# Performance work log

Measured on AMD Instinct MI355X. Metric: run time of the kernel, lower is better.

Reference implementation:

```python
import jax, jax.numpy as jnp
import numpy as np

D = 128          # data_dim
H = 512          # hidden_dim
K = 10           # num_bins
BATCH = 32768
BOUND = 5.0
MINW = 1e-3
MINH = 1e-3
MIND = 1e-3
MASK = np.array([1.0] * (D // 2) + [0.0] * (D // 2), dtype=np.float32)
TIDX = np.where(MASK == 0)[0]  # transformed dims (static)


def _rqs_forward(x, uw, uh, ud):
    # x: [B, T]; uw/uh: [B, T, K]; ud: [B, T, K-1]
    w = jax.nn.softmax(uw, axis=-1)
    w = MINW + (1.0 - MINW * K) * w
    cw = jnp.pad(jnp.cumsum(w, axis=-1), ((0, 0), (0, 0), (1, 0)))
    cw = 2.0 * BOUND * cw - BOUND
    cw = cw.at[..., 0].set(-BOUND).at[..., -1].set(BOUND)
    w = cw[..., 1:] - cw[..., :-1]

    h = jax.nn.softmax(uh, axis=-1)
    h = MINH + (1.0 - MINH * K) * h
    ch = jnp.pad(jnp.cumsum(h, axis=-1), ((0, 0), (0, 0), (1, 0)))
    ch = 2.0 * BOUND * ch - BOUND
    ch = ch.at[..., 0].set(-BOUND).at[..., -1].set(BOUND)
    h = ch[..., 1:] - ch[..., :-1]

    d = MIND + jax.nn.softplus(ud)
    d = jnp.pad(d, ((0, 0), (0, 0), (1, 1)), constant_values=1.0)  # [B,T,K+1]

    inside = (x >= -BOUND) & (x <= BOUND)
    xc = jnp.clip(x, -BOUND, BOUND)  # avoid NaN for outside values

    # searchsorted(cw, x, right=True) - 1, clamped to [0, K-1]
    bin_idx = jnp.clip(jnp.sum(cw <= xc[..., None], axis=-1) - 1, 0, K - 1)

    def gat(a, idx):
        return jnp.take_along_axis(a, idx[..., None], axis=-1)[..., 0]

    wk = gat(w, bin_idx)
    cwk = gat(cw, bin_idx)
    hk = gat(h, bin_idx)
    chk = gat(ch, bin_idx)
    dk = gat(d, bin_idx)
    dk1 = gat(d, bin_idx + 1)

    theta = (xc - cwk) / wk
    s = hk / wk
    tm = theta * (1.0 - theta)
    den = s + (dk + dk1 - 2.0 * s) * tm
    num = hk * (s * theta * theta + dk * tm)
    y = chk + num / den
    ld = jnp.log(s * s * (dk1 * theta * theta + 2.0 * s * tm + dk * (1.0 - theta) ** 2)) - 2.0 * jnp.log(den)

    y = jnp.where(inside, y, x)
    ld = jnp.where(inside, ld, 0.0)
    return y, ld


def setup_inputs() -> dict:
    key = jax.random.key(0)
    ks = jax.random.split(key, 7)
    out_dim = D * (3 * K - 1)
    return {
        "z": jax.random.normal(ks[0], (BATCH, D), dtype=jnp.float32) * 2.0,
        "W1": jax.random.normal(ks[1], (H, D), dtype=jnp.float32) * 0.05,
        "b1": jnp.zeros((H,), dtype=jnp.float32),
        "W2": jax.random.normal(ks[2], (H, H), dtype=jnp.float32) * 0.05,
        "b2": jnp.zeros((H,), dtype=jnp.float32),
        "W3": jax.random.normal(ks[3], (out_dim, H), dtype=jnp.float32) * 0.05,
        "b3": jnp.zeros((out_dim,), dtype=jnp.float32),
    }


def reference(z, W1, b1, W2, b2, W3, b3):
    mask = jnp.asarray(MASK)
    z_a = z * mask
    hdn = jax.nn.relu(z_a @ W1.T + b1)
    hdn = jax.nn.relu(hdn @ W2.T + b2)
    p = (hdn @ W3.T + b3).reshape(-1, D, 3 * K - 1)
    uw, uh, ud = jnp.split(p, [K, 2 * K], axis=-1)

    zb = z[:, TIDX]
    xb, ld = _rqs_forward(zb, uw[:, TIDX], uh[:, TIDX], ud[:, TIDX])

    x = z.at[:, TIDX].set(xb)
    logdet = jnp.sum(ld, axis=1)
    x = jnp.where(jnp.isnan(x) | jnp.isinf(x), 0.0, x)
    logdet = jnp.where(jnp.isnan(logdet) | jnp.isinf(logdet), 0.0, logdet)
    return x, logdet
```

## Files before the change

kernel.cpp:

```cpp
#include <hip/hip_runtime.h>
#include <cmath>

#define BATCH 32768
#define DIM   128
#define HID   512
#define NPAD  2048

typedef __attribute__((ext_vector_type(8))) _Float16 half8;
typedef __attribute__((ext_vector_type(8))) short   short8v;
typedef __attribute__((ext_vector_type(4))) float   f32x4;
typedef unsigned short u16;


__device__ __forceinline__ u16 f2h(float f) {
  _Float16 h = (_Float16)f;
  union { _Float16 h; u16 u; } v; v.h = h; return v.u;
}

__device__ __forceinline__ void async16(const void* g, void* l) {
  __builtin_amdgcn_global_load_lds(
      (const __attribute__((address_space(1))) void*)g,
      (__attribute__((address_space(3))) void*)l, 16, 0, 0);
}

__device__ __forceinline__ int xcd_swz(int bid, int nwg) {
  int cpx = nwg >> 3;
  return (bid & 7) * cpx + (bid >> 3);
}


__global__ __launch_bounds__(256) void prep_all_v8(
    const float* __restrict__ z, const float* __restrict__ W1, const float* __restrict__ W2,
    const float* __restrict__ W3, const float* __restrict__ b3,
    u16* __restrict__ zh, u16* __restrict__ W1h, u16* __restrict__ W2h,
    u16* __restrict__ W3h, float* __restrict__ b3p) {
  const int bid = blockIdx.x;
  if (bid < 1024) {
    int id = bid * 256 + threadIdx.x;
    int l = id & 63, mb = (id >> 6) & 2047, kt = id >> 17;
    int r = mb * 16 + (l & 15);
    int k0 = kt * 32 + ((l >> 4) << 3);
    const float* src = z + (size_t)r * DIM + k0;
    short8v H;
#pragma unroll
    for (int j = 0; j < 8; ++j) H[j] = (short)f2h(src[j]);
    *(short8v*)(zh + (size_t)id * 8) = H;
  } else if (bid < 1168) {
    int id = (bid - 1024) * 256 + threadIdx.x;
    if (id < 4096) {
      int l = id & 63, mb = (id >> 6) & 31, kt = id >> 11;
      int r = mb * 16 + (l & 15);
      int k0 = kt * 32 + ((l >> 4) << 3);
      const float* src = W1 + (size_t)r * DIM + k0;
      short8v H;
#pragma unroll
      for (int j = 0; j < 8; ++j) H[j] = (short)f2h(src[j]);
      *(short8v*)(W1h + (size_t)id * 8) = H;
    } else {
      int id2 = id - 4096;
      int l = id2 & 63, mb = (id2 >> 6) & 31, kt = id2 >> 11;
      int r = mb * 16 + (l & 15);
      int k0 = kt * 32 + ((l >> 4) << 3);
      const float* src = W2 + (size_t)r * HID + k0;
      short8v H;
#pragma unroll
      for (int j = 0; j < 8; ++j) H[j] = (short)f2h(src[j]);
      *(short8v*)(W2h + (size_t)id2 * 8) = H;
    }
  } else if (bid < 1680) {
    int id = (bid - 1168) * 256 + threadIdx.x;
    int l = id & 63, mb = (id >> 6) & 127, kt = id >> 13;
    int n = mb * 16 + (l & 15);
    int k0 = kt * 32 + ((l >> 4) << 3);
    int g = n >> 5, kk = n & 31;
    short8v H;
    if (kk < 29) {
      const float* src = W3 + ((size_t)((g + 64) * 29 + kk)) * HID + k0;
#pragma unroll
      for (int j = 0; j < 8; ++j) H[j] = (short)f2h(src[j]);
    } else {
#pragma unroll
      for (int j = 0; j < 8; ++j) H[j] = 0;
    }
    *(short8v*)(W3h + (size_t)id * 8) = H;
  } else {
    int n = (bid - 1680) * 256 + threadIdx.x;
    int g = n >> 5, kk = n & 31;
    b3p[n] = (kk < 29) ? b3[(g + 64) * 29 + kk] : 0.f;
  }
}


__device__ __forceinline__ void stageA_v8(const u16* __restrict__ A, size_t ab, u16* Lb, int t) {
  async16(A + ab + t * 8,         Lb + t * 8);
  async16(A + ab + (t + 256) * 8, Lb + (t + 256) * 8);
}

template<int NKT>
__device__ __forceinline__ void gemm_mainloop_v8(
    const u16* __restrict__ A, const u16* __restrict__ B,
    int a_rb0, int a_rs16, int b_rb0, int b_rs16,
    u16* LDS, f32x4 acc[4][4]) {
  const int t = threadIdx.x;
  const int lane = t & 63;
  const int wv = t >> 6;
  const int wr = wv >> 1, wc = wv & 1;
  const size_t aStep = (size_t)a_rs16 * 512;
  const size_t bStep = (size_t)b_rs16 * 512;
  const size_t ab0 = (size_t)a_rb0 * 512;
  const u16* Bbase = B + (((size_t)(b_rb0 + wc * 4)) * 64 + lane) * 8;

  half8 breg[2][4];
#pragma unroll
  for (int nf = 0; nf < 4; ++nf)
    breg[0][nf] = *(const half8*)(Bbase + nf * 512);
  stageA_v8(A, ab0, LDS, t);
  if (NKT > 1) stageA_v8(A, ab0 + aStep, LDS + 4096, t);

#pragma unroll
  for (int kt = 0; kt < NKT; ++kt) {
    if (kt + 1 < NKT) {
#pragma unroll
      for (int nf = 0; nf < 4; ++nf)
        breg[(kt + 1) & 1][nf] = *(const half8*)(Bbase + (size_t)(kt + 1) * bStep + nf * 512);
    }
    if (kt + 2 < NKT)
      stageA_v8(A, ab0 + (size_t)(kt + 2) * aStep, LDS + ((kt + 2) & 3) * 4096, t);
    if (kt + 2 < NKT)      asm volatile("s_waitcnt vmcnt(8)" ::: "memory");
    else if (kt + 1 < NKT) asm volatile("s_waitcnt vmcnt(6)" ::: "memory");
    else                   asm volatile("s_waitcnt vmcnt(0)" ::: "memory");
    __builtin_amdgcn_s_barrier();
    __builtin_amdgcn_sched_barrier(0);
    half8 a[4];
#pragma unroll
    for (int mf = 0; mf < 4; ++mf)
      a[mf] = *(const half8*)(LDS + (kt & 3) * 4096 + ((wr * 4 + mf) * 64 + lane) * 8);
#pragma unroll
    for (int mf = 0; mf < 4; ++mf)
#pragma unroll
      for (int nf = 0; nf < 4; ++nf)
        acc[mf][nf] = __builtin_amdgcn_mfma_f32_16x16x32_f16(a[mf], breg[kt & 1][nf], acc[mf][nf], 0, 0, 0);
  }
}


template<int NKT>
__global__ __launch_bounds__(256, 3) void gemm_relu_v8(
    const u16* __restrict__ A, const u16* __restrict__ B,
    const float* __restrict__ bias, u16* __restrict__ C, int a_rs16) {
  __shared__ __align__(16) u16 LDS[16384];
  const int bid = xcd_swz(blockIdx.x, gridDim.x);
  const int nt = bid & 3;
  const int mt = bid >> 2;
  const int m0 = mt << 7, n0 = nt << 7;
  f32x4 zero = {0.f, 0.f, 0.f, 0.f};
  f32x4 acc[4][4];
#pragma unroll
  for (int i = 0; i < 4; ++i)
#pragma unroll
    for (int j = 0; j < 4; ++j) acc[i][j] = zero;

  gemm_mainloop_v8<NKT>(A, B, m0 >> 4, a_rs16, n0 >> 4, 32, LDS, acc);

  const int lane = threadIdx.x & 63;
  const int wv = threadIdx.x >> 6;
  const int wr = wv >> 1, wc = wv & 1;
#pragma unroll
  for (int mf = 0; mf < 4; ++mf) {
#pragma unroll
    for (int nf = 0; nf < 4; ++nf) {
      int col = n0 + wc * 64 + nf * 16 + (lane & 15);
      float bv = bias[col];
#pragma unroll
      for (int r = 0; r < 4; ++r) {
        int row = m0 + wr * 64 + mf * 16 + (lane >> 4) * 4 + r;
        float v = fmaxf(acc[mf][nf][r] + bv, 0.f);
        int ktO = col >> 5, mbO = row >> 4;
        int lO = (row & 15) | (((col >> 3) & 3) << 4);
        int jO = col & 7;
        size_t off = (((size_t)ktO * (BATCH >> 4) + mbO) * 64 + lO) * 8 + jO;
        C[off] = f2h(v);
      }
    }
  }
}


__device__ __forceinline__ void rqs(float xin, const float uw[10], const float uh[10], const float ud9[9],
                                    float& yv, float& ldv) {
  float mw = uw[0];
#pragma unroll
  for (int i = 1; i < 10; ++i) mw = fmaxf(mw, uw[i]);
  float ew[10]; float sw = 0.f;
#pragma unroll
  for (int i = 0; i < 10; ++i) { ew[i] = __expf(uw[i] - mw); sw += ew[i]; }
  float invw = 0.99f / sw;
  float cw[11]; cw[0] = -5.f;
  {
    float run = 0.f;
#pragma unroll
    for (int i = 0; i < 10; ++i) { run += 0.001f + invw * ew[i]; cw[i + 1] = 10.f * run - 5.f; }
  }
  cw[10] = 5.f;
  float mh = uh[0];
#pragma unroll
  for (int i = 1; i < 10; ++i) mh = fmaxf(mh, uh[i]);
  float eh[10]; float sh = 0.f;
#pragma unroll
  for (int i = 0; i < 10; ++i) { eh[i] = __expf(uh[i] - mh); sh += eh[i]; }
  float invh = 0.99f / sh;
  float ch[11]; ch[0] = -5.f;
  {
    float run = 0.f;
#pragma unroll
    for (int i = 0; i < 10; ++i) { run += 0.001f + invh * eh[i]; ch[i + 1] = 10.f * run - 5.f; }
  }
  ch[10] = 5.f;
  float dv[11]; dv[0] = 1.f; dv[10] = 1.f;
#pragma unroll
  for (int i = 0; i < 9; ++i) {
    float x = ud9[i];
    float sp = fmaxf(x, 0.f) + __logf(1.f + __expf(-fabsf(x)));
    dv[i + 1] = 0.001f + sp;
  }

  float xc = fminf(fmaxf(xin, -5.f), 5.f);
  int b = 0;
#pragma unroll
  for (int j = 1; j <= 10; ++j) b += (cw[j] <= xc) ? 1 : 0;
  b = (b > 9) ? 9 : b;

  float wk = cw[1] - cw[0], cwk = cw[0], hk = ch[1] - ch[0], chk = ch[0], dk = dv[0], dk1 = dv[1];
#pragma unroll
  for (int j = 1; j < 10; ++j) {
    if (j == b) { wk = cw[j + 1] - cw[j]; cwk = cw[j]; hk = ch[j + 1] - ch[j]; chk = ch[j]; dk = dv[j]; dk1 = dv[j + 1]; }
  }

  float th = (xc - cwk) / wk;
  float sr = hk / wk;
  float omth = 1.f - th;
  float tm = th * omth;
  float den = sr + (dk + dk1 - 2.f * sr) * tm;
  float num = hk * (sr * th * th + dk * tm);
  float y = chk + num / den;
  float ld = __logf(sr * sr * (dk1 * th * th + 2.f * sr * tm + dk * omth * omth)) - 2.f * __logf(den);
  bool inside = (xin >= -5.f) && (xin <= 5.f);
  yv = inside ? y : xin;
  ldv = inside ? ld : 0.f;
  if (!isfinite(yv)) yv = 0.f;
}


__global__ __launch_bounds__(256, 3) void gemm3_spline_v8(
    const u16* __restrict__ A, const u16* __restrict__ B,
    const float* __restrict__ b3p, const float* __restrict__ z,
    float* __restrict__ xout, float* __restrict__ partial) {
  __shared__ __align__(16) char SMEM[33792];
  u16* LDS = (u16*)SMEM;
  float* PTf = (float*)SMEM;
  const int bid = xcd_swz(blockIdx.x, gridDim.x);
  const int nt = bid & 15;
  const int mt = bid >> 4;
  const int m0 = mt << 7, n0 = nt << 7;
  f32x4 zero = {0.f, 0.f, 0.f, 0.f};
  f32x4 acc[4][4];
#pragma unroll
  for (int i = 0; i < 4; ++i)
#pragma unroll
    for (int j = 0; j < 4; ++j) acc[i][j] = zero;

  gemm_mainloop_v8<16>(A, B, m0 >> 4, BATCH >> 4, n0 >> 4, NPAD >> 4, LDS, acc);

  const int t = threadIdx.x;
  const int lane = t & 63;
  const int wv = t >> 6;
  const int wr = wv >> 1, wc = wv & 1;
  const int gb = n0 >> 5;

  for (int p = 0; p < 2; ++p) {
    __syncthreads();
    if (wr == p) {
#pragma unroll
      for (int mf = 0; mf < 4; ++mf)
#pragma unroll
        for (int nf = 0; nf < 4; ++nf)
#pragma unroll
          for (int r = 0; r < 4; ++r) {
            int cl = wc * 64 + nf * 16 + (lane & 15);
            int rowl = mf * 16 + (lane >> 4) * 4 + r;
            PTf[rowl * 132 + (cl >> 5) * 33 + (cl & 31)] = acc[mf][nf][r];
          }
    }
    __syncthreads();

    const int rl = t >> 2;
    const int g = t & 3;
    const int row = p * 64 + rl;
    const int grow = m0 + row;
    const float* pr = PTf + rl * 132 + g * 33;
    const float* bb = b3p + n0 + g * 32;
    float uw[10], uh[10], ud9[9];
#pragma unroll
    for (int i = 0; i < 10; ++i) uw[i] = pr[i] + bb[i];
#pragma unroll
    for (int i = 0; i < 10; ++i) uh[i] = pr[10 + i] + bb[10 + i];
#pragma unroll
    for (int i = 0; i < 9; ++i) ud9[i] = pr[20 + i] + bb[20 + i];

    float xin = z[(long)grow * DIM + 64 + gb + g];
    float yv, ldv;
    rqs(xin, uw, uh, ud9, yv, ldv);

    xout[(long)grow * DIM + 64 + gb + g] = yv;

    float s = ldv;
    s += __shfl_down(s, 1);
    s += __shfl_down(s, 2);
    if (g == 0) partial[(long)nt * BATCH + grow] = s;
  }
}


__global__ __launch_bounds__(256) void copy_first_v8(const float* __restrict__ z, float* __restrict__ xout) {
  int id = blockIdx.x * 256 + threadIdx.x;
  int m = id >> 4, c4 = id & 15;
  const float4 v = *(const float4*)(z + (long)m * DIM + c4 * 4);
  *(float4*)(xout + (long)m * DIM + c4 * 4) = v;
}

__global__ __launch_bounds__(256) void reduce_ld_v8(const float* __restrict__ partial, float* __restrict__ ldout) {
  int row = blockIdx.x * 256 + threadIdx.x;
  float s = 0.f;
#pragma unroll
  for (int i = 0; i < 16; ++i) s += partial[(long)i * BATCH + row];
  if (!isfinite(s)) s = 0.f;
  ldout[row] = s;
}


extern "C" void kernel_launch(void* const* d_in, const int* in_sizes, int n_in,
                              void* d_out, int out_size, void* d_ws, size_t ws_size,
                              hipStream_t stream) {
  const float* z  = (const float*)d_in[0];
  const float* W1 = (const float*)d_in[1];
  const float* b1 = (const float*)d_in[2];
  const float* W2 = (const float*)d_in[3];
  const float* b2 = (const float*)d_in[4];
  const float* W3 = (const float*)d_in[5];
  const float* b3 = (const float*)d_in[6];
  float* xout  = (float*)d_out;
  float* ldout = xout + (size_t)BATCH * DIM;

  char* ws = (char*)d_ws;
  u16* W1h = (u16*)ws;  ws += (size_t)512 * 64 * 2;
  u16* W2h = (u16*)ws;  ws += (size_t)512 * 512 * 2;
  u16* W3h = (u16*)ws;  ws += (size_t)NPAD * HID * 2;
  float* b3p = (float*)ws; ws += (size_t)NPAD * 4;
  u16* zah  = (u16*)ws;
  float* part = (float*)ws; ws += (size_t)BATCH * 64 * 2;
  u16* h1h = (u16*)ws;  ws += (size_t)BATCH * HID * 2;
  u16* h2h = (u16*)ws;  ws += (size_t)BATCH * HID * 2;

  prep_all_v8<<<1688, 256, 0, stream>>>(z, W1, W2, W3, b3, zah, W1h, W2h, W3h, b3p);

  gemm_relu_v8<2><<<(BATCH / 128) * 4, 256, 0, stream>>>(zah, W1h, b1, h1h, BATCH >> 4);
  gemm_relu_v8<16><<<(BATCH / 128) * 4, 256, 0, stream>>>(h1h, W2h, b2, h2h, BATCH >> 4);
  gemm3_spline_v8<<<(BATCH / 128) * (NPAD / 128), 256, 0, stream>>>(h2h, W3h, b3p, z, xout, part);

  copy_first_v8<<<(BATCH * 16) / 256, 256, 0, stream>>>(z, xout);
  reduce_ld_v8<<<BATCH / 256, 256, 0, stream>>>(part, ldout);
}
```

Baseline: 150.5 us.

## Load GEMM A fragments directly to registers instead of async LDS staging

Drops the global_load_lds staging of A tiles through LDS, along with the manual vmcnt waits and barriers. Each wave now loads its A and B fragments straight into double-buffered registers from the pre-swizzled layout. This removes per-k-step barriers and LDS traffic. In exchange, A is loaded twice per block (once by each of the two column waves), which raises global/L2 traffic and register pressure.

```diff
diff --git a/kernel.cpp b/kernel.cpp
--- a/kernel.cpp
+++ b/kernel.cpp
@@ -17,19 +17,13 @@
   union { _Float16 h; u16 u; } v; v.h = h; return v.u;
 }
 
-__device__ __forceinline__ void async16(const void* g, void* l) {
-  __builtin_amdgcn_global_load_lds(
-      (const __attribute__((address_space(1))) void*)g,
-      (__attribute__((address_space(3))) void*)l, 16, 0, 0);
-}
-
 __device__ __forceinline__ int xcd_swz(int bid, int nwg) {
   int cpx = nwg >> 3;
   return (bid & 7) * cpx + (bid >> 3);
 }
 
 
-__global__ __launch_bounds__(256) void prep_all_v8(
+__global__ __launch_bounds__(256) void prep_all_v11(
     const float* __restrict__ z, const float* __restrict__ W1, const float* __restrict__ W2,
     const float* __restrict__ W3, const float* __restrict__ b3,
     u16* __restrict__ zh, u16* __restrict__ W1h, u16* __restrict__ W2h,
@@ -91,64 +85,47 @@
 }
 
 
-__device__ __forceinline__ void stageA_v8(const u16* __restrict__ A, size_t ab, u16* Lb, int t) {
-  async16(A + ab + t * 8,         Lb + t * 8);
-  async16(A + ab + (t + 256) * 8, Lb + (t + 256) * 8);
-}
-
 template<int NKT>
-__device__ __forceinline__ void gemm_mainloop_v8(
+__device__ __forceinline__ void gemm_mainloop_v11(
     const u16* __restrict__ A, const u16* __restrict__ B,
-    int a_rb0, int a_rs16, int b_rb0, int b_rs16,
-    u16* LDS, f32x4 acc[4][4]) {
-  const int t = threadIdx.x;
-  const int lane = t & 63;
-  const int wv = t >> 6;
+    int a_mb0, int a_rs16, int b_nb0, int b_rs16, f32x4 acc[4][4]) {
+  const int lane = threadIdx.x & 63;
+  const int wv = threadIdx.x >> 6;
   const int wr = wv >> 1, wc = wv & 1;
   const size_t aStep = (size_t)a_rs16 * 512;
   const size_t bStep = (size_t)b_rs16 * 512;
-  const size_t ab0 = (size_t)a_rb0 * 512;
-  const u16* Bbase = B + (((size_t)(b_rb0 + wc * 4)) * 64 + lane) * 8;
-
-  half8 breg[2][4];
-#pragma unroll
-  for (int nf = 0; nf < 4; ++nf)
-    breg[0][nf] = *(const half8*)(Bbase + nf * 512);
-  stageA_v8(A, ab0, LDS, t);
-  if (NKT > 1) stageA_v8(A, ab0 + aStep, LDS + 4096, t);
-
+  const u16* Ap = A + (((size_t)(a_mb0 + wr * 4)) * 64 + lane) * 8;
+  const u16* Bp = B + (((size_t)(b_nb0 + wc * 4)) * 64 + lane) * 8;
+
+  half8 a[2][4], b[2][4];
+#pragma unroll
+  for (int f = 0; f < 4; ++f) {
+    a[0][f] = *(const half8*)(Ap + f * 512);
+    b[0][f] = *(const half8*)(Bp + f * 512);
+  }
 #pragma unroll
   for (int kt = 0; kt < NKT; ++kt) {
+    const int cur = kt & 1, nxt = cur ^ 1;
     if (kt + 1 < NKT) {
 #pragma unroll
+      for (int f = 0; f < 4; ++f) {
+        a[nxt][f] = *(const half8*)(Ap + (size_t)(kt + 1) * aStep + f * 512);
+        b[nxt][f] = *(const half8*)(Bp + (size_t)(kt + 1) * bStep + f * 512);
+      }
+    }
+#pragma unroll
+    for (int mf = 0; mf < 4; ++mf)
+#pragma unroll
       for (int nf = 0; nf < 4; ++nf)
-        breg[(kt + 1) & 1][nf] = *(const half8*)(Bbase + (size_t)(kt + 1) * bStep + nf * 512);
-    }
-    if (kt + 2 < NKT)
-      stageA_v8(A, ab0 + (size_t)(kt + 2) * aStep, LDS + ((kt + 2) & 3) * 4096, t);
-    if (kt + 2 < NKT)      asm volatile("s_waitcnt vmcnt(8)" ::: "memory");
-    else if (kt + 1 < NKT) asm volatile("s_waitcnt vmcnt(6)" ::: "memory");
-    else                   asm volatile("s_waitcnt vmcnt(0)" ::: "memory");
-    __builtin_amdgcn_s_barrier();
-    __builtin_amdgcn_sched_barrier(0);
-    half8 a[4];
-#pragma unroll
-    for (int mf = 0; mf < 4; ++mf)
-      a[mf] = *(const half8*)(LDS + (kt & 3) * 4096 + ((wr * 4 + mf) * 64 + lane) * 8);
-#pragma unroll
-    for (int mf = 0; mf < 4; ++mf)
-#pragma unroll
-      for (int nf = 0; nf < 4; ++nf)
-        acc[mf][nf] = __builtin_amdgcn_mfma_f32_16x16x32_f16(a[mf], breg[kt & 1][nf], acc[mf][nf], 0, 0, 0);
+        acc[mf][nf] = __builtin_amdgcn_mfma_f32_16x16x32_f16(a[cur][mf], b[cur][nf], acc[mf][nf], 0, 0, 0);
   }
 }
 
 
 template<int NKT>
-__global__ __launch_bounds__(256, 3) void gemm_relu_v8(
+__global__ __launch_bounds__(256, 3) void gemm_relu_v11(
     const u16* __restrict__ A, const u16* __restrict__ B,
     const float* __restrict__ bias, u16* __restrict__ C, int a_rs16) {
-  __shared__ __align__(16) u16 LDS[16384];
   const int bid = xcd_swz(blockIdx.x, gridDim.x);
   const int nt = bid & 3;
   const int mt = bid >> 2;
@@ -160,7 +137,7 @@
 #pragma unroll
     for (int j = 0; j < 4; ++j) acc[i][j] = zero;
 
-  gemm_mainloop_v8<NKT>(A, B, m0 >> 4, a_rs16, n0 >> 4, 32, LDS, acc);
+  gemm_mainloop_v11<NKT>(A, B, m0 >> 4, a_rs16, n0 >> 4, 32, acc);
 
   const int lane = threadIdx.x & 63;
   const int wv = threadIdx.x >> 6;
@@ -251,13 +228,11 @@
 }
 
 
-__global__ __launch_bounds__(256, 3) void gemm3_spline_v8(
+__global__ __launch_bounds__(256, 3) void gemm3_spline_v11(
     const u16* __restrict__ A, const u16* __restrict__ B,
     const float* __restrict__ b3p, const float* __restrict__ z,
     float* __restrict__ xout, float* __restrict__ partial) {
-  __shared__ __align__(16) char SMEM[33792];
-  u16* LDS = (u16*)SMEM;
-  float* PTf = (float*)SMEM;
+  __shared__ __align__(16) float PTf[64 * 132];
   const int bid = xcd_swz(blockIdx.x, gridDim.x);
   const int nt = bid & 15;
   const int mt = bid >> 4;
@@ -269,7 +244,7 @@
 #pragma unroll
     for (int j = 0; j < 4; ++j) acc[i][j] = zero;
 
-  gemm_mainloop_v8<16>(A, B, m0 >> 4, BATCH >> 4, n0 >> 4, NPAD >> 4, LDS, acc);
+  gemm_mainloop_v11<16>(A, B, m0 >> 4, BATCH >> 4, n0 >> 4, NPAD >> 4, acc);
 
   const int t = threadIdx.x;
   const int lane = t & 63;
@@ -321,14 +296,14 @@
 }
 
 
-__global__ __launch_bounds__(256) void copy_first_v8(const float* __restrict__ z, float* __restrict__ xout) {
+__global__ __launch_bounds__(256) void copy_first_v11(const float* __restrict__ z, float* __restrict__ xout) {
   int id = blockIdx.x * 256 + threadIdx.x;
   int m = id >> 4, c4 = id & 15;
   const float4 v = *(const float4*)(z + (long)m * DIM + c4 * 4);
   *(float4*)(xout + (long)m * DIM + c4 * 4) = v;
 }
 
-__global__ __launch_bounds__(256) void reduce_ld_v8(const float* __restrict__ partial, float* __restrict__ ldout) {
+__global__ __launch_bounds__(256) void reduce_ld_v11(const float* __restrict__ partial, float* __restrict__ ldout) {
   int row = blockIdx.x * 256 + threadIdx.x;
   float s = 0.f;
 #pragma unroll
@@ -361,12 +336,12 @@
   u16* h1h = (u16*)ws;  ws += (size_t)BATCH * HID * 2;
   u16* h2h = (u16*)ws;  ws += (size_t)BATCH * HID * 2;
 
-  prep_all_v8<<<1688, 256, 0, stream>>>(z, W1, W2, W3, b3, zah, W1h, W2h, W3h, b3p);
-
-  gemm_relu_v8<2><<<(BATCH / 128) * 4, 256, 0, stream>>>(zah, W1h, b1, h1h, BATCH >> 4);
-  gemm_relu_v8<16><<<(BATCH / 128) * 4, 256, 0, stream>>>(h1h, W2h, b2, h2h, BATCH >> 4);
-  gemm3_spline_v8<<<(BATCH / 128) * (NPAD / 128), 256, 0, stream>>>(h2h, W3h, b3p, z, xout, part);
-
-  copy_first_v8<<<(BATCH * 16) / 256, 256, 0, stream>>>(z, xout);
-  reduce_ld_v8<<<BATCH / 256, 256, 0, stream>>>(part, ldout);
-}
+  prep_all_v11<<<1688, 256, 0, stream>>>(z, W1, W2, W3, b3, zah, W1h, W2h, W3h, b3p);
+
+  gemm_relu_v11<2><<<(BATCH / 128) * 4, 256, 0, stream>>>(zah, W1h, b1, h1h, BATCH >> 4);
+  gemm_relu_v11<16><<<(BATCH / 128) * 4, 256, 0, stream>>>(h1h, W2h, b2, h2h, BATCH >> 4);
+  gemm3_spline_v11<<<(BATCH / 128) * (NPAD / 128), 256, 0, stream>>>(h2h, W3h, b3p, z, xout, part);
+
+  copy_first_v11<<<(BATCH * 16) / 256, 256, 0, stream>>>(z, xout);
+  reduce_ld_v11<<<BATCH / 256, 256, 0, stream>>>(part, ldout);
+}
```

Result: slower. 172.5 us (+14.7%).

## Widen GEMM block tiles to 128x256 with 64x128 per-wave output

Applied to the files above, without the earlier changes.

Each wave's output tile doubles along N: it now keeps 8 B fragments double-buffered in registers and 32 accumulators. The grids for all three GEMMs are halved and occupancy hints drop from 3 to 2 blocks per CU. The spline epilogue now walks four 64x128 sub-tiles, one per wave, with the ld partial index adjusted to match. The goal is to halve how often A tiles are re-streamed through LDS and to raise MFMA work per load. In exchange register pressure and occupancy get worse, and the new vmcnt thresholds (4/2) are stricter than needed, which reduces load/compute overlap.

```diff
diff --git a/kernel.cpp b/kernel.cpp
--- a/kernel.cpp
+++ b/kernel.cpp
@@ -23,13 +23,21 @@
       (__attribute__((address_space(3))) void*)l, 16, 0, 0);
 }
 
+__device__ __forceinline__ void vwait(int n) {
+  switch (n) {
+    case 0:  asm volatile("s_waitcnt vmcnt(0)" ::: "memory"); break;
+    case 2:  asm volatile("s_waitcnt vmcnt(2)" ::: "memory"); break;
+    default: asm volatile("s_waitcnt vmcnt(4)" ::: "memory"); break;
+  }
+}
+
 __device__ __forceinline__ int xcd_swz(int bid, int nwg) {
   int cpx = nwg >> 3;
   return (bid & 7) * cpx + (bid >> 3);
 }
 
 
-__global__ __launch_bounds__(256) void prep_all_v8(
+__global__ __launch_bounds__(256) void prep_all_v13(
     const float* __restrict__ z, const float* __restrict__ W1, const float* __restrict__ W2,
     const float* __restrict__ W3, const float* __restrict__ b3,
     u16* __restrict__ zh, u16* __restrict__ W1h, u16* __restrict__ W2h,
@@ -91,44 +99,43 @@
 }
 
 
-__device__ __forceinline__ void stageA_v8(const u16* __restrict__ A, size_t ab, u16* Lb, int t) {
+__device__ __forceinline__ void stageA_v13(const u16* __restrict__ A, size_t ab, u16* Lb, int t) {
   async16(A + ab + t * 8,         Lb + t * 8);
   async16(A + ab + (t + 256) * 8, Lb + (t + 256) * 8);
 }
 
 template<int NKT>
-__device__ __forceinline__ void gemm_mainloop_v8(
+__device__ __forceinline__ void gemm_mainloop_v13(
     const u16* __restrict__ A, const u16* __restrict__ B,
-    int a_rb0, int a_rs16, int b_rb0, int b_rs16,
-    u16* LDS, f32x4 acc[4][4]) {
+    int a_mb0, int a_rs16, int b_nb0, int b_rs16,
+    u16* LDS, f32x4 acc[4][8]) {
   const int t = threadIdx.x;
   const int lane = t & 63;
   const int wv = t >> 6;
   const int wr = wv >> 1, wc = wv & 1;
   const size_t aStep = (size_t)a_rs16 * 512;
   const size_t bStep = (size_t)b_rs16 * 512;
-  const size_t ab0 = (size_t)a_rb0 * 512;
-  const u16* Bbase = B + (((size_t)(b_rb0 + wc * 4)) * 64 + lane) * 8;
-
-  half8 breg[2][4];
-#pragma unroll
-  for (int nf = 0; nf < 4; ++nf)
-    breg[0][nf] = *(const half8*)(Bbase + nf * 512);
-  stageA_v8(A, ab0, LDS, t);
-  if (NKT > 1) stageA_v8(A, ab0 + aStep, LDS + 4096, t);
+  const size_t ab0 = (size_t)a_mb0 * 512;
+  const u16* Bp = B + (((size_t)(b_nb0 + wc * 8)) * 64 + lane) * 8;
+
+  half8 b[2][8];
+#pragma unroll
+  for (int nf = 0; nf < 8; ++nf) b[0][nf] = *(const half8*)(Bp + nf * 512);
+  stageA_v13(A, ab0, LDS, t);
+  if (NKT > 1) stageA_v13(A, ab0 + aStep, LDS + 4096, t);
 
 #pragma unroll
   for (int kt = 0; kt < NKT; ++kt) {
     if (kt + 1 < NKT) {
 #pragma unroll
-      for (int nf = 0; nf < 4; ++nf)
-        breg[(kt + 1) & 1][nf] = *(const half8*)(Bbase + (size_t)(kt + 1) * bStep + nf * 512);
+      for (int nf = 0; nf < 8; ++nf)
+        b[(kt + 1) & 1][nf] = *(const half8*)(Bp + (size_t)(kt + 1) * bStep + nf * 512);
     }
     if (kt + 2 < NKT)
-      stageA_v8(A, ab0 + (size_t)(kt + 2) * aStep, LDS + ((kt + 2) & 3) * 4096, t);
-    if (kt + 2 < NKT)      asm volatile("s_waitcnt vmcnt(8)" ::: "memory");
-    else if (kt + 1 < NKT) asm volatile("s_waitcnt vmcnt(6)" ::: "memory");
-    else                   asm volatile("s_waitcnt vmcnt(0)" ::: "memory");
+      stageA_v13(A, ab0 + (size_t)(kt + 2) * aStep, LDS + ((kt + 2) & 3) * 4096, t);
+    if (kt + 2 < NKT)      vwait(4);
+    else if (kt + 1 < NKT) vwait(2);
+    else                   vwait(0);
     __builtin_amdgcn_s_barrier();
     __builtin_amdgcn_sched_barrier(0);
     half8 a[4];
@@ -138,29 +145,29 @@
 #pragma unroll
     for (int mf = 0; mf < 4; ++mf)
 #pragma unroll
-      for (int nf = 0; nf < 4; ++nf)
-        acc[mf][nf] = __builtin_amdgcn_mfma_f32_16x16x32_f16(a[mf], breg[kt & 1][nf], acc[mf][nf], 0, 0, 0);
-  }
-}
-
-
-template<int NKT>
-__global__ __launch_bounds__(256, 3) void gemm_relu_v8(
+      for (int nf = 0; nf < 8; ++nf)
+        acc[mf][nf] = __builtin_amdgcn_mfma_f32_16x16x32_f16(a[mf], b[kt & 1][nf], acc[mf][nf], 0, 0, 0);
+  }
+}
+
+
+template<int NKT, int NTL>
+__global__ __launch_bounds__(256, 2) void gemm_relu_v13(
     const u16* __restrict__ A, const u16* __restrict__ B,
     const float* __restrict__ bias, u16* __restrict__ C, int a_rs16) {
   __shared__ __align__(16) u16 LDS[16384];
   const int bid = xcd_swz(blockIdx.x, gridDim.x);
-  const int nt = bid & 3;
-  const int mt = bid >> 2;
-  const int m0 = mt << 7, n0 = nt << 7;
+  const int nt = bid & ((1 << NTL) - 1);
+  const int mt = bid >> NTL;
+  const int m0 = mt << 7, n0 = nt << 8;
   f32x4 zero = {0.f, 0.f, 0.f, 0.f};
-  f32x4 acc[4][4];
+  f32x4 acc[4][8];
 #pragma unroll
   for (int i = 0; i < 4; ++i)
 #pragma unroll
-    for (int j = 0; j < 4; ++j) acc[i][j] = zero;
-
-  gemm_mainloop_v8<NKT>(A, B, m0 >> 4, a_rs16, n0 >> 4, 32, LDS, acc);
+    for (int j = 0; j < 8; ++j) acc[i][j] = zero;
+
+  gemm_mainloop_v13<NKT>(A, B, m0 >> 4, a_rs16, n0 >> 4, 32, LDS, acc);
 
   const int lane = threadIdx.x & 63;
   const int wv = threadIdx.x >> 6;
@@ -168,8 +175,8 @@
 #pragma unroll
   for (int mf = 0; mf < 4; ++mf) {
 #pragma unroll
-    for (int nf = 0; nf < 4; ++nf) {
-      int col = n0 + wc * 64 + nf * 16 + (lane & 15);
+    for (int nf = 0; nf < 8; ++nf) {
+      int col = n0 + wc * 128 + nf * 16 + (lane & 15);
       float bv = bias[col];
 #pragma unroll
       for (int r = 0; r < 4; ++r) {
@@ -251,7 +258,7 @@
 }
 
 
-__global__ __launch_bounds__(256, 3) void gemm3_spline_v8(
+__global__ __launch_bounds__(256, 2) void gemm3_spline_v13(
     const u16* __restrict__ A, const u16* __restrict__ B,
     const float* __restrict__ b3p, const float* __restrict__ z,
     float* __restrict__ xout, float* __restrict__ partial) {
@@ -259,46 +266,47 @@
   u16* LDS = (u16*)SMEM;
   float* PTf = (float*)SMEM;
   const int bid = xcd_swz(blockIdx.x, gridDim.x);
-  const int nt = bid & 15;
-  const int mt = bid >> 4;
-  const int m0 = mt << 7, n0 = nt << 7;
+  const int nt = bid & 7;
+  const int mt = bid >> 3;
+  const int m0 = mt << 7, n0 = nt << 8;
   f32x4 zero = {0.f, 0.f, 0.f, 0.f};
-  f32x4 acc[4][4];
+  f32x4 acc[4][8];
 #pragma unroll
   for (int i = 0; i < 4; ++i)
 #pragma unroll
-    for (int j = 0; j < 4; ++j) acc[i][j] = zero;
-
-  gemm_mainloop_v8<16>(A, B, m0 >> 4, BATCH >> 4, n0 >> 4, NPAD >> 4, LDS, acc);
+    for (int j = 0; j < 8; ++j) acc[i][j] = zero;
+
+  gemm_mainloop_v13<16>(A, B, m0 >> 4, BATCH >> 4, n0 >> 4, NPAD >> 4, LDS, acc);
 
   const int t = threadIdx.x;
   const int lane = t & 63;
   const int wv = t >> 6;
   const int wr = wv >> 1, wc = wv & 1;
-  const int gb = n0 >> 5;
-
-  for (int p = 0; p < 2; ++p) {
+
+#pragma unroll
+  for (int s = 0; s < 4; ++s) {
+    const int s_r = s >> 1, s_c = s & 1;
     __syncthreads();
-    if (wr == p) {
+    if (wr == s_r && wc == s_c) {
 #pragma unroll
       for (int mf = 0; mf < 4; ++mf)
 #pragma unroll
-        for (int nf = 0; nf < 4; ++nf)
+        for (int nf = 0; nf < 8; ++nf)
 #pragma unroll
           for (int r = 0; r < 4; ++r) {
-            int cl = wc * 64 + nf * 16 + (lane & 15);
+            int cp = nf * 16 + (lane & 15);
             int rowl = mf * 16 + (lane >> 4) * 4 + r;
-            PTf[rowl * 132 + (cl >> 5) * 33 + (cl & 31)] = acc[mf][nf][r];
+            PTf[rowl * 132 + (cp >> 5) * 33 + (cp & 31)] = acc[mf][nf][r];
           }
     }
     __syncthreads();
 
-    const int rl = t >> 2;
-    const int g = t & 3;
-    const int row = p * 64 + rl;
-    const int grow = m0 + row;
-    const float* pr = PTf + rl * 132 + g * 33;
-    const float* bb = b3p + n0 + g * 32;
+    const int row = t >> 2;
+    const int g4 = t & 3;
+    const int grow = m0 + s_r * 64 + row;
+    const int gdim = (n0 >> 5) + s_c * 4 + g4;
+    const float* pr = PTf + row * 132 + g4 * 33;
+    const float* bb = b3p + n0 + s_c * 128 + g4 * 32;
     float uw[10], uh[10], ud9[9];
 #pragma unroll
     for (int i = 0; i < 10; ++i) uw[i] = pr[i] + bb[i];
@@ -307,28 +315,29 @@
 #pragma unroll
     for (int i = 0; i < 9; ++i) ud9[i] = pr[20 + i] + bb[20 + i];
 
-    float xin = z[(long)grow * DIM + 64 + gb + g];
+    float xin = z[(long)grow * DIM + 64 + gdim];
     float yv, ldv;
     rqs(xin, uw, uh, ud9, yv, ldv);
 
-    xout[(long)grow * DIM + 64 + gb + g] = yv;
-
-    float s = ldv;
-    s += __shfl_down(s, 1);
-    s += __shfl_down(s, 2);
-    if (g == 0) partial[(long)nt * BATCH + grow] = s;
-  }
-}
-
-
-__global__ __launch_bounds__(256) void copy_first_v8(const float* __restrict__ z, float* __restrict__ xout) {
+    xout[(long)grow * DIM + 64 + gdim] = yv;
+
+    float sld = ldv;
+    sld += __shfl_down(sld, 1);
+    sld += __shfl_down(sld, 2);
+    if (g4 == 0)
+      partial[(size_t)(nt * 2 + s_c) * BATCH + grow] = sld;
+  }
+}
+
+
+__global__ __launch_bounds__(256) void copy_first_v13(const float* __restrict__ z, float* __restrict__ xout) {
   int id = blockIdx.x * 256 + threadIdx.x;
   int m = id >> 4, c4 = id & 15;
   const float4 v = *(const float4*)(z + (long)m * DIM + c4 * 4);
   *(float4*)(xout + (long)m * DIM + c4 * 4) = v;
 }
 
-__global__ __launch_bounds__(256) void reduce_ld_v8(const float* __restrict__ partial, float* __restrict__ ldout) {
+__global__ __launch_bounds__(256) void reduce_ld_v13(const float* __restrict__ partial, float* __restrict__ ldout) {
   int row = blockIdx.x * 256 + threadIdx.x;
   float s = 0.f;
 #pragma unroll
@@ -361,12 +370,12 @@
   u16* h1h = (u16*)ws;  ws += (size_t)BATCH * HID * 2;
   u16* h2h = (u16*)ws;  ws += (size_t)BATCH * HID * 2;
 
-  prep_all_v8<<<1688, 256, 0, stream>>>(z, W1, W2, W3, b3, zah, W1h, W2h, W3h, b3p);
-
-  gemm_relu_v8<2><<<(BATCH / 128) * 4, 256, 0, stream>>>(zah, W1h, b1, h1h, BATCH >> 4);
-  gemm_relu_v8<16><<<(BATCH / 128) * 4, 256, 0, stream>>>(h1h, W2h, b2, h2h, BATCH >> 4);
-  gemm3_spline_v8<<<(BATCH / 128) * (NPAD / 128), 256, 0, stream>>>(h2h, W3h, b3p, z, xout, part);
-
-  copy_first_v8<<<(BATCH * 16) / 256, 256, 0, stream>>>(z, xout);
-  reduce_ld_v8<<<BATCH / 256, 256, 0, stream>>>(part, ldout);
-}
+  prep_all_v13<<<1688, 256, 0, stream>>>(z, W1, W2, W3, b3, zah, W1h, W2h, W3h, b3p);
+
+  gemm_relu_v13<2, 1><<<(BATCH / 128) * 2, 256, 0, stream>>>(zah, W1h, b1, h1h, BATCH >> 4);
+  gemm_relu_v13<16, 1><<<(BATCH / 128) * 2, 256, 0, stream>>>(h1h, W2h, b2, h2h, BATCH >> 4);
+  gemm3_spline_v13<<<(BATCH / 128) * (NPAD / 256), 256, 0, stream>>>(h2h, W3h, b3p, z, xout, part);
+
+  copy_first_v13<<<(BATCH * 16) / 256, 256, 0, stream>>>(z, xout);
+  reduce_ld_v13<<<BATCH / 256, 256, 0, stream>>>(part, ldout);
+}
```

Result: slower. 163.3 us (+8.5%).

## Process two k-tiles per barrier with triple-buffered LDS in GEMM mainloop

Applied to the files above, without the earlier changes.

Restructures the shared GEMM mainloop so each barrier phase covers two k-tiles, with LDS split into three buffers of two tiles each. Prefetch of the next phase's A tiles is issued before a single waitcnt and barrier. This halves the number of workgroup barriers and waitcnt stalls per k-loop while keeping B double-buffered in registers. In exchange, LDS per block grows to 48KB, which may limit how many blocks share a CU, and the prefetch lead becomes coarser.

```diff
diff --git a/kernel.cpp b/kernel.cpp
--- a/kernel.cpp
+++ b/kernel.cpp
@@ -23,13 +23,20 @@
       (__attribute__((address_space(3))) void*)l, 16, 0, 0);
 }
 
+__device__ __forceinline__ void vwait(int n) {
+  switch (n) {
+    case 0:  asm volatile("s_waitcnt vmcnt(0)" ::: "memory"); break;
+    default: asm volatile("s_waitcnt vmcnt(4)" ::: "memory"); break;
+  }
+}
+
 __device__ __forceinline__ int xcd_swz(int bid, int nwg) {
   int cpx = nwg >> 3;
   return (bid & 7) * cpx + (bid >> 3);
 }
 
 
-__global__ __launch_bounds__(256) void prep_all_v8(
+__global__ __launch_bounds__(256) void prep_all_v14(
     const float* __restrict__ z, const float* __restrict__ W1, const float* __restrict__ W2,
     const float* __restrict__ W3, const float* __restrict__ b3,
     u16* __restrict__ zh, u16* __restrict__ W1h, u16* __restrict__ W2h,
@@ -91,64 +98,72 @@
 }
 
 
-__device__ __forceinline__ void stageA_v8(const u16* __restrict__ A, size_t ab, u16* Lb, int t) {
+__device__ __forceinline__ void stageA_v14(const u16* __restrict__ A, size_t ab, u16* Lb, int t) {
   async16(A + ab + t * 8,         Lb + t * 8);
   async16(A + ab + (t + 256) * 8, Lb + (t + 256) * 8);
 }
 
 template<int NKT>
-__device__ __forceinline__ void gemm_mainloop_v8(
+__device__ __forceinline__ void gemm_mainloop_v14(
     const u16* __restrict__ A, const u16* __restrict__ B,
-    int a_rb0, int a_rs16, int b_rb0, int b_rs16,
+    int a_mb0, int a_rs16, int b_nb0, int b_rs16,
     u16* LDS, f32x4 acc[4][4]) {
+  constexpr int NPH = NKT / 2;
   const int t = threadIdx.x;
   const int lane = t & 63;
   const int wv = t >> 6;
   const int wr = wv >> 1, wc = wv & 1;
   const size_t aStep = (size_t)a_rs16 * 512;
   const size_t bStep = (size_t)b_rs16 * 512;
-  const size_t ab0 = (size_t)a_rb0 * 512;
-  const u16* Bbase = B + (((size_t)(b_rb0 + wc * 4)) * 64 + lane) * 8;
-
-  half8 breg[2][4];
-#pragma unroll
-  for (int nf = 0; nf < 4; ++nf)
-    breg[0][nf] = *(const half8*)(Bbase + nf * 512);
-  stageA_v8(A, ab0, LDS, t);
-  if (NKT > 1) stageA_v8(A, ab0 + aStep, LDS + 4096, t);
-
-#pragma unroll
-  for (int kt = 0; kt < NKT; ++kt) {
-    if (kt + 1 < NKT) {
-#pragma unroll
-      for (int nf = 0; nf < 4; ++nf)
-        breg[(kt + 1) & 1][nf] = *(const half8*)(Bbase + (size_t)(kt + 1) * bStep + nf * 512);
-    }
-    if (kt + 2 < NKT)
-      stageA_v8(A, ab0 + (size_t)(kt + 2) * aStep, LDS + ((kt + 2) & 3) * 4096, t);
-    if (kt + 2 < NKT)      asm volatile("s_waitcnt vmcnt(8)" ::: "memory");
-    else if (kt + 1 < NKT) asm volatile("s_waitcnt vmcnt(6)" ::: "memory");
-    else                   asm volatile("s_waitcnt vmcnt(0)" ::: "memory");
+  const size_t ab0 = (size_t)a_mb0 * 512;
+  const u16* Bp = B + (((size_t)(b_nb0 + wc * 4)) * 64 + lane) * 8;
+
+  half8 b[2][4];
+#pragma unroll
+  for (int nf = 0; nf < 4; ++nf) b[0][nf] = *(const half8*)(Bp + nf * 512);
+  stageA_v14(A, ab0, LDS, t);
+  stageA_v14(A, ab0 + aStep, LDS + 4096, t);
+
+#pragma unroll
+  for (int p = 0; p < NPH; ++p) {
+    if (p + 1 < NPH) {
+      u16* pb = LDS + ((p + 1) % 3) * 8192;
+      stageA_v14(A, ab0 + (size_t)(2 * p + 2) * aStep, pb, t);
+      stageA_v14(A, ab0 + (size_t)(2 * p + 3) * aStep, pb + 4096, t);
+      vwait(4);
+    } else {
+      vwait(0);
+    }
     __builtin_amdgcn_s_barrier();
     __builtin_amdgcn_sched_barrier(0);
-    half8 a[4];
-#pragma unroll
-    for (int mf = 0; mf < 4; ++mf)
-      a[mf] = *(const half8*)(LDS + (kt & 3) * 4096 + ((wr * 4 + mf) * 64 + lane) * 8);
-#pragma unroll
-    for (int mf = 0; mf < 4; ++mf)
-#pragma unroll
-      for (int nf = 0; nf < 4; ++nf)
-        acc[mf][nf] = __builtin_amdgcn_mfma_f32_16x16x32_f16(a[mf], breg[kt & 1][nf], acc[mf][nf], 0, 0, 0);
+    const u16* cb = LDS + (p % 3) * 8192;
+#pragma unroll
+    for (int ktl = 0; ktl < 2; ++ktl) {
+      const int kt = 2 * p + ktl;
+      if (kt + 1 < NKT) {
+#pragma unroll
+        for (int nf = 0; nf < 4; ++nf)
+          b[(kt + 1) & 1][nf] = *(const half8*)(Bp + (size_t)(kt + 1) * bStep + nf * 512);
+      }
+      half8 a[4];
+#pragma unroll
+      for (int mf = 0; mf < 4; ++mf)
+        a[mf] = *(const half8*)(cb + ktl * 4096 + ((wr * 4 + mf) * 64 + lane) * 8);
+#pragma unroll
+      for (int mf = 0; mf < 4; ++mf)
+#pragma unroll
+        for (int nf = 0; nf < 4; ++nf)
+          acc[mf][nf] = __builtin_amdgcn_mfma_f32_16x16x32_f16(a[mf], b[kt & 1][nf], acc[mf][nf], 0, 0, 0);
+    }
   }
 }
 
 
 template<int NKT>
-__global__ __launch_bounds__(256, 3) void gemm_relu_v8(
+__global__ __launch_bounds__(256, 3) void gemm_relu_v14(
     const u16* __restrict__ A, const u16* __restrict__ B,
     const float* __restrict__ bias, u16* __restrict__ C, int a_rs16) {
-  __shared__ __align__(16) u16 LDS[16384];
+  __shared__ __align__(16) u16 LDS[24576];
   const int bid = xcd_swz(blockIdx.x, gridDim.x);
   const int nt = bid & 3;
   const int mt = bid >> 2;
@@ -160,7 +175,7 @@
 #pragma unroll
     for (int j = 0; j < 4; ++j) acc[i][j] = zero;
 
-  gemm_mainloop_v8<NKT>(A, B, m0 >> 4, a_rs16, n0 >> 4, 32, LDS, acc);
+  gemm_mainloop_v14<NKT>(A, B, m0 >> 4, a_rs16, n0 >> 4, 32, LDS, acc);
 
   const int lane = threadIdx.x & 63;
   const int wv = threadIdx.x >> 6;
@@ -251,11 +266,11 @@
 }
 
 
-__global__ __launch_bounds__(256, 3) void gemm3_spline_v8(
+__global__ __launch_bounds__(256, 3) void gemm3_spline_v14(
     const u16* __restrict__ A, const u16* __restrict__ B,
     const float* __restrict__ b3p, const float* __restrict__ z,
     float* __restrict__ xout, float* __restrict__ partial) {
-  __shared__ __align__(16) char SMEM[33792];
+  __shared__ __align__(16) char SMEM[49152];
   u16* LDS = (u16*)SMEM;
   float* PTf = (float*)SMEM;
   const int bid = xcd_swz(blockIdx.x, gridDim.x);
@@ -269,7 +284,7 @@
 #pragma unroll
     for (int j = 0; j < 4; ++j) acc[i][j] = zero;
 
-  gemm_mainloop_v8<16>(A, B, m0 >> 4, BATCH >> 4, n0 >> 4, NPAD >> 4, LDS, acc);
+  gemm_mainloop_v14<16>(A, B, m0 >> 4, BATCH >> 4, n0 >> 4, NPAD >> 4, LDS, acc);
 
   const int t = threadIdx.x;
   const int lane = t & 63;
@@ -321,14 +336,14 @@
 }
 
 
-__global__ __launch_bounds__(256) void copy_first_v8(const float* __restrict__ z, float* __restrict__ xout) {
+__global__ __launch_bounds__(256) void copy_first_v14(const float* __restrict__ z, float* __restrict__ xout) {
   int id = blockIdx.x * 256 + threadIdx.x;
   int m = id >> 4, c4 = id & 15;
   const float4 v = *(const float4*)(z + (long)m * DIM + c4 * 4);
   *(float4*)(xout + (long)m * DIM + c4 * 4) = v;
 }
 
-__global__ __launch_bounds__(256) void reduce_ld_v8(const float* __restrict__ partial, float* __restrict__ ldout) {
+__global__ __launch_bounds__(256) void reduce_ld_v14(const float* __restrict__ partial, float* __restrict__ ldout) {
   int row = blockIdx.x * 256 + threadIdx.x;
   float s = 0.f;
 #pragma unroll
@@ -361,12 +376,12 @@
   u16* h1h = (u16*)ws;  ws += (size_t)BATCH * HID * 2;
   u16* h2h = (u16*)ws;  ws += (size_t)BATCH * HID * 2;
 
-  prep_all_v8<<<1688, 256, 0, stream>>>(z, W1, W2, W3, b3, zah, W1h, W2h, W3h, b3p);
-
-  gemm_relu_v8<2><<<(BATCH / 128) * 4, 256, 0, stream>>>(zah, W1h, b1, h1h, BATCH >> 4);
-  gemm_relu_v8<16><<<(BATCH / 128) * 4, 256, 0, stream>>>(h1h, W2h, b2, h2h, BATCH >> 4);
-  gemm3_spline_v8<<<(BATCH / 128) * (NPAD / 128), 256, 0, stream>>>(h2h, W3h, b3p, z, xout, part);
-
-  copy_first_v8<<<(BATCH * 16) / 256, 256, 0, stream>>>(z, xout);
-  reduce_ld_v8<<<BATCH / 256, 256, 0, stream>>>(part, ldout);
-}
+  prep_all_v14<<<1688, 256, 0, stream>>>(z, W1, W2, W3, b3, zah, W1h, W2h, W3h, b3p);
+
+  gemm_relu_v14<2><<<(BATCH / 128) * 4, 256, 0, stream>>>(zah, W1h, b1, h1h, BATCH >> 4);
+  gemm_relu_v14<16><<<(BATCH / 128) * 4, 256, 0, stream>>>(h1h, W2h, b2, h2h, BATCH >> 4);
+  gemm3_spline_v14<<<(BATCH / 128) * (NPAD / 128), 256, 0, stream>>>(h2h, W3h, b3p, z, xout, part);
+
+  copy_first_v14<<<(BATCH * 16) / 256, 256, 0, stream>>>(z, xout);
+  reduce_ld_v14<<<BATCH / 256, 256, 0, stream>>>(part, ldout);
+}
```

New measurement: 153.3 us. No clear change (+1.9%).
